# Optimization experiments

Measured on AMD Instinct MI355X. Metric: run time of the kernel, lower is better.

The kernel has to match this reference:

```python
import jax, jax.numpy as jnp
import numpy as np

B, T, IN, H, L, OUT = 1024, 48, 64, 512, 3, 1


def setup_inputs() -> dict:
    key = jax.random.key(0)
    ks = jax.random.split(key, 12)
    s = 0.05
    inp = {
        "x": jax.random.normal(ks[0], (B, T, IN), dtype=jnp.float32),
        # layer 0: input IN -> H ; gates concatenated [f,i,c,o] along last dim
        "Wx0": jax.random.normal(ks[1], (IN, 4 * H), dtype=jnp.float32) * s,
        "Wh0": jax.random.normal(ks[2], (H, 4 * H), dtype=jnp.float32) * s,
        "b0": jnp.zeros((4 * H,), dtype=jnp.float32),
        "Wx1": jax.random.normal(ks[3], (H, 4 * H), dtype=jnp.float32) * s,
        "Wh1": jax.random.normal(ks[4], (H, 4 * H), dtype=jnp.float32) * s,
        "b1": jnp.zeros((4 * H,), dtype=jnp.float32),
        "Wx2": jax.random.normal(ks[5], (H, 4 * H), dtype=jnp.float32) * s,
        "Wh2": jax.random.normal(ks[6], (H, 4 * H), dtype=jnp.float32) * s,
        "b2": jnp.zeros((4 * H,), dtype=jnp.float32),
        "fc_w": jax.random.normal(ks[7], (H, OUT), dtype=jnp.float32) * s,
        "fc_b": jnp.zeros((OUT,), dtype=jnp.float32),
    }
    return inp


def _lstm_cell(Wx, Wh, b, x_t, h, C):
    # fused 4-gate GEMM, same math as 8 separate Linears in the torch code
    g = x_t @ Wx + h @ Wh + b  # [B, 4H]
    f, i, c, o = jnp.split(g, 4, axis=-1)
    f = jax.nn.sigmoid(f)
    i = jax.nn.sigmoid(i)
    c = jnp.tanh(c)
    o = jax.nn.sigmoid(o)
    C_new = f * C + i * c
    h_new = o * jnp.tanh(C_new)  # dropout is identity in eval mode
    return h_new, C_new


def reference(x, Wx0, Wh0, b0, Wx1, Wh1, b1, Wx2, Wh2, b2, fc_w, fc_b):
    params = [(Wx0, Wh0, b0), (Wx1, Wh1, b1), (Wx2, Wh2, b2)]
    Bsz = x.shape[0]
    Hsz = Wh0.shape[0]
    h0 = jnp.zeros((L, Bsz, Hsz), dtype=x.dtype)
    C0 = jnp.zeros((L, Bsz, Hsz), dtype=x.dtype)

    def step(carry, x_t):
        h, C = carry
        inp = x_t
        hs, Cs = [], []
        for l in range(L):
            Wx, Wh, b = params[l]
            hn, Cn = _lstm_cell(Wx, Wh, b, inp, h[l], C[l])
            hs.append(hn)
            Cs.append(Cn)
            inp = hn
        return (jnp.stack(hs), jnp.stack(Cs)), None

    (h, C), _ = jax.lax.scan(step, (h0, C0), jnp.swapaxes(x, 0, 1))
    return h[-1] @ fc_w + fc_b  # [B, OUT]
```

## Files before the change

kernel.cpp:

```cpp
#include <hip/hip_runtime.h>
#include <hip/hip_bf16.h>
#include <stdint.h>

#define BSZ 1024
#define HSZ 512
#define TSZ 48
#define INSZ 64
#define GSZ 2048

typedef __attribute__((ext_vector_type(8))) short bf16x8;
typedef __attribute__((ext_vector_type(16))) float f32x16;

#define GLDS16(g, l)                                                        \
    __builtin_amdgcn_global_load_lds(                                       \
        (const __attribute__((address_space(1))) void*)(g),                 \
        (__attribute__((address_space(3))) void*)(l), 16, 0, 0)

__device__ __forceinline__ float sigmf(float x) { return 1.0f / (1.0f + __expf(-x)); }
__device__ __forceinline__ float tanhf_(float x) { return 2.0f / (1.0f + __expf(-2.0f * x)) - 1.0f; }

__global__ __launch_bounds__(256, 3) void lstm_diag(
    const __hip_bfloat16* __restrict__ xth, const __hip_bfloat16* __restrict__ xtl,
    __hip_bfloat16* __restrict__ hbuf,
    float* __restrict__ Cbuf,
    const __hip_bfloat16* __restrict__ W0h, const __hip_bfloat16* __restrict__ W0l,
    const __hip_bfloat16* __restrict__ W1h, const __hip_bfloat16* __restrict__ W1l,
    const __hip_bfloat16* __restrict__ W2h, const __hip_bfloat16* __restrict__ W2l,
    const float* __restrict__ b0, const float* __restrict__ b1,
    const float* __restrict__ b2,
    int d, int lmin)
{
    __shared__ __align__(16) char lds[49152];
    char* ldsAh = lds;
    char* ldsAl = lds + 8192;
    char* ldsBh = lds + 16384;
    char* ldsBl = lds + 32768;

    const int l = lmin + blockIdx.z;
    const int t = d - l;
    const size_t slab = (size_t)BSZ * HSZ;
    auto Hb = [&](int par, int ll, int hilo) {
        return hbuf + (((size_t)par * 3 + ll) * 2 + hilo) * slab;
    };

    const __hip_bfloat16* Wth = (l == 0) ? W0h : (l == 1) ? W1h : W2h;
    const __hip_bfloat16* Wtl = (l == 0) ? W0l : (l == 1) ? W1l : W2l;
    const float* bias = (l == 0) ? b0 : (l == 1) ? b1 : b2;
    const int Kx   = (l == 0) ? INSZ : HSZ;
    const int KCax = (l == 0) ? 8 : 64;
    const int Ktot = Kx + HSZ;
    const int KCt  = Ktot >> 3;
    const int nkx  = Kx >> 6;
    const int nkt  = Ktot >> 6;
    const int cur = t & 1, prv = cur ^ 1;
    const __hip_bfloat16* Axh = (l == 0) ? xth + (size_t)t * BSZ * INSZ : Hb(cur, l - 1, 0);
    const __hip_bfloat16* Axl = (l == 0) ? xtl + (size_t)t * BSZ * INSZ : Hb(cur, l - 1, 1);
    const __hip_bfloat16* Ahh = Hb(prv, l, 0);
    const __hip_bfloat16* Ahl = Hb(prv, l, 1);
    float* C = Cbuf + (size_t)l * slab;
    __hip_bfloat16* hhi = Hb(cur, l, 0);
    __hip_bfloat16* hlo = Hb(cur, l, 1);

    const int bid = blockIdx.x + (blockIdx.y << 4);
    const int swz = (bid & 7) * 32 + (bid >> 3);
    const int m0 = (swz & 15) * 64;
    const int n0 = (swz >> 4) * 128;
    const int p  = swz & 15;
    const int np = swz >> 4;

    const int tid = threadIdx.x;
    const int lane = tid & 63;
    const int wv = tid >> 6;
    const int lrow32 = lane & 31;
    const int lk2 = lane >> 5;

    int offA[2][4], offB[4];
#pragma unroll
    for (int mf = 0; mf < 2; ++mf)
#pragma unroll
        for (int ks = 0; ks < 4; ++ks)
            offA[mf][ks] = (ks * 2 + lk2) * 1024 + (mf * 32 + lrow32) * 16;
#pragma unroll
    for (int ks = 0; ks < 4; ++ks)
        offB[ks] = (ks * 2 + lk2) * 2048 + (wv * 32 + lrow32) * 16;

    f32x16 acc[2];
#pragma unroll
    for (int mf = 0; mf < 2; ++mf)
#pragma unroll
        for (int r = 0; r < 16; ++r) acc[mf][r] = 0.0f;

    auto stage = [&](const __hip_bfloat16* sh, const __hip_bfloat16* sl,
                     int KCa, int kcA0, int kcW0) {
#pragma unroll
        for (int i = 0; i < 2; ++i) {
            int sa = wv * 2 + i;
            size_t ro = ((size_t)p * KCa + kcA0 + sa) * 512 + lane * 8;
            GLDS16(sh + ro, ldsAh + sa * 1024);
            GLDS16(sl + ro, ldsAl + sa * 1024);
        }
#pragma unroll
        for (int i = 0; i < 4; ++i) {
            int sb = wv * 4 + i;
            size_t ro = ((size_t)np * KCt + kcW0 + (sb >> 1)) * 1024 + (sb & 1) * 512 + lane * 8;
            GLDS16(Wth + ro, ldsBh + sb * 1024);
            GLDS16(Wtl + ro, ldsBl + sb * 1024);
        }
    };

#pragma unroll 1
    for (int ks = 0; ks < nkt; ++ks) {
        __syncthreads();
        if (ks < nkx) stage(Axh, Axl, KCax, ks * 8, ks * 8);
        else          stage(Ahh, Ahl, 64, (ks - nkx) * 8, ks * 8);
        __syncthreads();
#pragma unroll
        for (int ksub = 0; ksub < 4; ++ksub) {
            bf16x8 ah0 = *(const bf16x8*)(ldsAh + offA[0][ksub]);
            bf16x8 ah1 = *(const bf16x8*)(ldsAh + offA[1][ksub]);
            bf16x8 al0 = *(const bf16x8*)(ldsAl + offA[0][ksub]);
            bf16x8 al1 = *(const bf16x8*)(ldsAl + offA[1][ksub]);
            bf16x8 bh  = *(const bf16x8*)(ldsBh + offB[ksub]);
            bf16x8 bl  = *(const bf16x8*)(ldsBl + offB[ksub]);
            acc[0] = __builtin_amdgcn_mfma_f32_32x32x16_bf16(ah0, bh, acc[0], 0, 0, 0);
            acc[1] = __builtin_amdgcn_mfma_f32_32x32x16_bf16(ah1, bh, acc[1], 0, 0, 0);
            acc[0] = __builtin_amdgcn_mfma_f32_32x32x16_bf16(al0, bh, acc[0], 0, 0, 0);
            acc[1] = __builtin_amdgcn_mfma_f32_32x32x16_bf16(al1, bh, acc[1], 0, 0, 0);
            acc[0] = __builtin_amdgcn_mfma_f32_32x32x16_bf16(ah0, bl, acc[0], 0, 0, 0);
            acc[1] = __builtin_amdgcn_mfma_f32_32x32x16_bf16(ah1, bl, acc[1], 0, 0, 0);
        }
    }

    __syncthreads();
    float* gt = (float*)lds;
#pragma unroll
    for (int mf = 0; mf < 2; ++mf)
#pragma unroll
        for (int rg = 0; rg < 16; ++rg) {
            int row = mf * 32 + (rg & 3) + 8 * (rg >> 2) + 4 * lk2;
            gt[row * 132 + wv * 32 + lrow32] = acc[mf][rg];
        }
    __syncthreads();

    const int n_l = tid & 31;
    const int rb2 = (tid >> 5) * 8;
    const int n_g = (n0 >> 2) + n_l;
    const int kc_h = n_g >> 3, e_h = n_g & 7;
    const float bf = bias[n_g], bi = bias[HSZ + n_g];
    const float bc = bias[2 * HSZ + n_g], bo = bias[3 * HSZ + n_g];
#pragma unroll
    for (int r = 0; r < 8; ++r) {
        int row = rb2 + r;
        int rg = m0 + row;
        float4 g4 = *(const float4*)&gt[row * 132 + n_l * 4];
        float f = sigmf(g4.x + bf);
        float i_ = sigmf(g4.y + bi);
        float c_ = tanhf_(g4.z + bc);
        float o_ = sigmf(g4.w + bo);
        size_t cidx = (size_t)rg * HSZ + n_g;
        float Cn = f * C[cidx] + i_ * c_;
        C[cidx] = Cn;
        float hv = o_ * tanhf_(Cn);
        __hip_bfloat16 hh = __float2bfloat16(hv);
        size_t hidx = (((size_t)(rg >> 6) * 64 + kc_h) * 64 + (rg & 63)) * 8 + e_h;
        hhi[hidx] = hh;
        hlo[hidx] = __float2bfloat16(hv - __bfloat162float(hh));
    }
}

__global__ __launch_bounds__(256) void convert_x(const float* __restrict__ x,
                                                 __hip_bfloat16* __restrict__ xh,
                                                 __hip_bfloat16* __restrict__ xl)
{
    int gid = blockIdx.x * 256 + threadIdx.x;
    int kc = gid & 7;
    int rem = gid >> 3;
    int r = rem & 63; rem >>= 6;
    int pp = rem & 15;
    int t = rem >> 4;
    int b = pp * 64 + r;
    const float* src = x + ((size_t)b * TSZ + t) * INSZ + kc * 8;
    short hi8[8], lo8[8];
#pragma unroll
    for (int e = 0; e < 8; ++e) {
        float v = src[e];
        __hip_bfloat16 h = __float2bfloat16(v);
        hi8[e] = *(short*)&h;
        __hip_bfloat16 lo = __float2bfloat16(v - __bfloat162float(h));
        lo8[e] = *(short*)&lo;
    }
    size_t o = ((((size_t)t * 16 + pp) * 8 + kc) * 64 + r) * 8;
    *(bf16x8*)((__hip_bfloat16*)xh + o) = *(bf16x8*)hi8;
    *(bf16x8*)((__hip_bfloat16*)xl + o) = *(bf16x8*)lo8;
}

__global__ __launch_bounds__(256) void convert_w(
    const float* __restrict__ Wx, const float* __restrict__ Wh, int Kx, int Ktot,
    __hip_bfloat16* __restrict__ outh, __hip_bfloat16* __restrict__ outl)
{
    __shared__ float tile[64][129];
    const int kt = blockIdx.x, np = blockIdx.y;
    const int k0 = kt * 64;
    const float* src;
    int krel;
    if (k0 < Kx) { src = Wx; krel = k0; } else { src = Wh; krel = k0 - Kx; }
#pragma unroll
    for (int i = 0; i < 32; ++i) {
        int idx = threadIdx.x + i * 256;
        int k_l = idx >> 7, gate = (idx >> 5) & 3, n_l = idx & 31;
        tile[k_l][n_l * 4 + gate] = src[(size_t)(krel + k_l) * GSZ + gate * HSZ + np * 32 + n_l];
    }
    __syncthreads();
    const size_t obase = ((size_t)np * (Ktot >> 3) + kt * 8) * 1024;
#pragma unroll
    for (int i = 0; i < 32; ++i) {
        int idx = threadIdx.x + i * 256;
        int kcl = idx >> 10, c = (idx >> 3) & 127, e = idx & 7;
        float v = tile[kcl * 8 + e][c];
        __hip_bfloat16 h = __float2bfloat16(v);
        outh[obase + idx] = h;
        outl[obase + idx] = __float2bfloat16(v - __bfloat162float(h));
    }
}

__global__ __launch_bounds__(256) void fc_kernel(
    const __hip_bfloat16* __restrict__ hh, const __hip_bfloat16* __restrict__ hl,
    const float* __restrict__ w, const float* __restrict__ b, float* __restrict__ out)
{
    int wave = (blockIdx.x * 256 + threadIdx.x) >> 6;
    int lane = threadIdx.x & 63;
    if (wave >= BSZ) return;
    int pp = wave >> 6, r = wave & 63;
    size_t o = (((size_t)pp * 64 + lane) * 64 + r) * 8;
    bf16x8 vh = *(const bf16x8*)(hh + o);
    bf16x8 vl = *(const bf16x8*)(hl + o);
    float s = 0.0f;
#pragma unroll
    for (int e = 0; e < 8; ++e) {
        ushort uh = (ushort)vh[e], ul = (ushort)vl[e];
        __hip_bfloat16 bh = *(__hip_bfloat16*)&uh;
        __hip_bfloat16 bl = *(__hip_bfloat16*)&ul;
        s += (__bfloat162float(bh) + __bfloat162float(bl)) * w[lane * 8 + e];
    }
#pragma unroll
    for (int off = 32; off; off >>= 1) s += __shfl_down(s, off);
    if (lane == 0) out[wave] = s + b[0];
}

extern "C" void kernel_launch(void* const* d_in, const int* in_sizes, int n_in,
                              void* d_out, int out_size, void* d_ws, size_t ws_size,
                              hipStream_t stream) {
    const float* x   = (const float*)d_in[0];
    const float* Wx0 = (const float*)d_in[1];
    const float* Wh0 = (const float*)d_in[2];
    const float* b0  = (const float*)d_in[3];
    const float* Wx1 = (const float*)d_in[4];
    const float* Wh1 = (const float*)d_in[5];
    const float* b1  = (const float*)d_in[6];
    const float* Wx2 = (const float*)d_in[7];
    const float* Wh2 = (const float*)d_in[8];
    const float* b2  = (const float*)d_in[9];
    const float* fcw = (const float*)d_in[10];
    const float* fcb = (const float*)d_in[11];

    char* p = (char*)d_ws;
    const size_t hslab = (size_t)BSZ * HSZ * sizeof(__hip_bfloat16);
    __hip_bfloat16* hbuf = (__hip_bfloat16*)p;
    p += 12 * hslab;
    float* Cbuf = (float*)p;
    p += 3 * (size_t)BSZ * HSZ * sizeof(float);
    const size_t zero_bytes = (size_t)(p - (char*)d_ws);

    const size_t xslab = (size_t)TSZ * BSZ * INSZ * sizeof(__hip_bfloat16);
    __hip_bfloat16* xth = (__hip_bfloat16*)p; p += xslab;
    __hip_bfloat16* xtl = (__hip_bfloat16*)p; p += xslab;

    const int K0 = INSZ + HSZ;
    const int K12 = 2 * HSZ;
    const size_t w0s = (size_t)GSZ * K0 * sizeof(__hip_bfloat16);
    const size_t w12s = (size_t)GSZ * K12 * sizeof(__hip_bfloat16);
    __hip_bfloat16* w0h = (__hip_bfloat16*)p; p += w0s;
    __hip_bfloat16* w0l = (__hip_bfloat16*)p; p += w0s;
    __hip_bfloat16* w1h = (__hip_bfloat16*)p; p += w12s;
    __hip_bfloat16* w1l = (__hip_bfloat16*)p; p += w12s;
    __hip_bfloat16* w2h = (__hip_bfloat16*)p; p += w12s;
    __hip_bfloat16* w2l = (__hip_bfloat16*)p; p += w12s;

    hipMemsetAsync(d_ws, 0, zero_bytes, stream);

    convert_x<<<dim3(TSZ * BSZ * 8 / 256), dim3(256), 0, stream>>>(x, xth, xtl);
    convert_w<<<dim3(K0 / 64, 16), dim3(256), 0, stream>>>(Wx0, Wh0, INSZ, K0, w0h, w0l);
    convert_w<<<dim3(K12 / 64, 16), dim3(256), 0, stream>>>(Wx1, Wh1, HSZ, K12, w1h, w1l);
    convert_w<<<dim3(K12 / 64, 16), dim3(256), 0, stream>>>(Wx2, Wh2, HSZ, K12, w2h, w2l);

    for (int dgn = 0; dgn < TSZ + 2; ++dgn) {
        int lmin = (dgn - (TSZ - 1)) > 0 ? (dgn - (TSZ - 1)) : 0;
        int lmax = dgn < 2 ? dgn : 2;
        int ncells = lmax - lmin + 1;
        lstm_diag<<<dim3(16, 16, ncells), dim3(256), 0, stream>>>(
            xth, xtl, hbuf, Cbuf,
            w0h, w0l, w1h, w1l, w2h, w2l,
            b0, b1, b2, dgn, lmin);
    }

    __hip_bfloat16* h2h = hbuf + (((size_t)1 * 3 + 2) * 2 + 0) * BSZ * HSZ;
    __hip_bfloat16* h2l = hbuf + (((size_t)1 * 3 + 2) * 2 + 1) * BSZ * HSZ;
    fc_kernel<<<dim3(BSZ / 4), dim3(256), 0, stream>>>(h2h, h2l, fcw, fcb, (float*)d_out);
}
```

Baseline: 2.042 ms.

## Replace LDS-staged GEMM mainloop with direct global-to-register prefetch pipeline

```diff
diff --git a/kernel.cpp b/kernel.cpp
--- a/kernel.cpp
+++ b/kernel.cpp
@@ -10,11 +10,6 @@
 
 typedef __attribute__((ext_vector_type(8))) short bf16x8;
 typedef __attribute__((ext_vector_type(16))) float f32x16;
-
-#define GLDS16(g, l)                                                        \
-    __builtin_amdgcn_global_load_lds(                                       \
-        (const __attribute__((address_space(1))) void*)(g),                 \
-        (__attribute__((address_space(3))) void*)(l), 16, 0, 0)
 
 __device__ __forceinline__ float sigmf(float x) { return 1.0f / (1.0f + __expf(-x)); }
 __device__ __forceinline__ float tanhf_(float x) { return 2.0f / (1.0f + __expf(-2.0f * x)) - 1.0f; }
@@ -30,11 +25,7 @@
     const float* __restrict__ b2,
     int d, int lmin)
 {
-    __shared__ __align__(16) char lds[49152];
-    char* ldsAh = lds;
-    char* ldsAl = lds + 8192;
-    char* ldsBh = lds + 16384;
-    char* ldsBl = lds + 32768;
+    __shared__ __align__(16) float gt[64 * 132];
 
     const int l = lmin + blockIdx.z;
     const int t = d - l;
@@ -50,8 +41,8 @@
     const int KCax = (l == 0) ? 8 : 64;
     const int Ktot = Kx + HSZ;
     const int KCt  = Ktot >> 3;
-    const int nkx  = Kx >> 6;
-    const int nkt  = Ktot >> 6;
+    const int qx   = Kx >> 4;
+    const int qtot = Ktot >> 4;
     const int cur = t & 1, prv = cur ^ 1;
     const __hip_bfloat16* Axh = (l == 0) ? xth + (size_t)t * BSZ * INSZ : Hb(cur, l - 1, 0);
     const __hip_bfloat16* Axl = (l == 0) ? xtl + (size_t)t * BSZ * INSZ : Hb(cur, l - 1, 1);
@@ -74,72 +65,64 @@
     const int lrow32 = lane & 31;
     const int lk2 = lane >> 5;
 
-    int offA[2][4], offB[4];
-#pragma unroll
-    for (int mf = 0; mf < 2; ++mf)
-#pragma unroll
-        for (int ks = 0; ks < 4; ++ks)
-            offA[mf][ks] = (ks * 2 + lk2) * 1024 + (mf * 32 + lrow32) * 16;
-#pragma unroll
-    for (int ks = 0; ks < 4; ++ks)
-        offB[ks] = (ks * 2 + lk2) * 2048 + (wv * 32 + lrow32) * 16;
-
-    f32x16 acc[2];
-#pragma unroll
-    for (int mf = 0; mf < 2; ++mf)
-#pragma unroll
-        for (int r = 0; r < 16; ++r) acc[mf][r] = 0.0f;
-
-    auto stage = [&](const __hip_bfloat16* sh, const __hip_bfloat16* sl,
-                     int KCa, int kcA0, int kcW0) {
-#pragma unroll
-        for (int i = 0; i < 2; ++i) {
-            int sa = wv * 2 + i;
-            size_t ro = ((size_t)p * KCa + kcA0 + sa) * 512 + lane * 8;
-            GLDS16(sh + ro, ldsAh + sa * 1024);
-            GLDS16(sl + ro, ldsAl + sa * 1024);
-        }
-#pragma unroll
-        for (int i = 0; i < 4; ++i) {
-            int sb = wv * 4 + i;
-            size_t ro = ((size_t)np * KCt + kcW0 + (sb >> 1)) * 1024 + (sb & 1) * 512 + lane * 8;
-            GLDS16(Wth + ro, ldsBh + sb * 1024);
-            GLDS16(Wtl + ro, ldsBl + sb * 1024);
-        }
-    };
+    const char* bAxh = (const char*)Axh + (size_t)p * KCax * 1024;
+    const char* bAxl = (const char*)Axl + (size_t)p * KCax * 1024;
+    const char* bAhh = (const char*)Ahh + (size_t)p * 64 * 1024;
+    const char* bAhl = (const char*)Ahl + (size_t)p * 64 * 1024;
+    const char* bWh  = (const char*)Wth + (size_t)np * KCt * 2048;
+    const char* bWl  = (const char*)Wtl + (size_t)np * KCt * 2048;
+
+    const int aoff = lk2 * 1024 + lrow32 * 16;
+    const int boff = lk2 * 2048 + (wv * 32 + lrow32) * 16;
+
+    f32x16 acc0, acc1;
+#pragma unroll
+    for (int r = 0; r < 16; ++r) { acc0[r] = 0.0f; acc1[r] = 0.0f; }
+
+    bf16x8 ah[4][2], al[4][2], bhv[4], blv[4];
+
+#define LOAD_SLOT(S, Q)                                                       \
+    { const int q_ = (Q);                                                     \
+      const char *pah, *pal;                                                  \
+      if (q_ < qx) { pah = bAxh + q_ * 2048; pal = bAxl + q_ * 2048; }        \
+      else { pah = bAhh + (q_ - qx) * 2048; pal = bAhl + (q_ - qx) * 2048; }  \
+      ah[S][0] = *(const bf16x8*)(pah + aoff);                                \
+      ah[S][1] = *(const bf16x8*)(pah + aoff + 512);                          \
+      al[S][0] = *(const bf16x8*)(pal + aoff);                                \
+      al[S][1] = *(const bf16x8*)(pal + aoff + 512);                          \
+      bhv[S] = __builtin_nontemporal_load((const bf16x8*)(bWh + q_ * 4096 + boff)); \
+      blv[S] = __builtin_nontemporal_load((const bf16x8*)(bWl + q_ * 4096 + boff)); }
+
+#define MMA_SLOT(S)                                                           \
+    acc0 = __builtin_amdgcn_mfma_f32_32x32x16_bf16(ah[S][0], bhv[S], acc0, 0, 0, 0); \
+    acc1 = __builtin_amdgcn_mfma_f32_32x32x16_bf16(ah[S][1], bhv[S], acc1, 0, 0, 0); \
+    acc0 = __builtin_amdgcn_mfma_f32_32x32x16_bf16(al[S][0], bhv[S], acc0, 0, 0, 0); \
+    acc1 = __builtin_amdgcn_mfma_f32_32x32x16_bf16(al[S][1], bhv[S], acc1, 0, 0, 0); \
+    acc0 = __builtin_amdgcn_mfma_f32_32x32x16_bf16(ah[S][0], blv[S], acc0, 0, 0, 0); \
+    acc1 = __builtin_amdgcn_mfma_f32_32x32x16_bf16(ah[S][1], blv[S], acc1, 0, 0, 0);
+
+    LOAD_SLOT(0, 0)
+    LOAD_SLOT(1, 1)
+    LOAD_SLOT(2, 2)
+    LOAD_SLOT(3, 3)
 
 #pragma unroll 1
-    for (int ks = 0; ks < nkt; ++ks) {
-        __syncthreads();
-        if (ks < nkx) stage(Axh, Axl, KCax, ks * 8, ks * 8);
-        else          stage(Ahh, Ahl, 64, (ks - nkx) * 8, ks * 8);
-        __syncthreads();
-#pragma unroll
-        for (int ksub = 0; ksub < 4; ++ksub) {
-            bf16x8 ah0 = *(const bf16x8*)(ldsAh + offA[0][ksub]);
-            bf16x8 ah1 = *(const bf16x8*)(ldsAh + offA[1][ksub]);
-            bf16x8 al0 = *(const bf16x8*)(ldsAl + offA[0][ksub]);
-            bf16x8 al1 = *(const bf16x8*)(ldsAl + offA[1][ksub]);
-            bf16x8 bh  = *(const bf16x8*)(ldsBh + offB[ksub]);
-            bf16x8 bl  = *(const bf16x8*)(ldsBl + offB[ksub]);
-            acc[0] = __builtin_amdgcn_mfma_f32_32x32x16_bf16(ah0, bh, acc[0], 0, 0, 0);
-            acc[1] = __builtin_amdgcn_mfma_f32_32x32x16_bf16(ah1, bh, acc[1], 0, 0, 0);
-            acc[0] = __builtin_amdgcn_mfma_f32_32x32x16_bf16(al0, bh, acc[0], 0, 0, 0);
-            acc[1] = __builtin_amdgcn_mfma_f32_32x32x16_bf16(al1, bh, acc[1], 0, 0, 0);
-            acc[0] = __builtin_amdgcn_mfma_f32_32x32x16_bf16(ah0, bl, acc[0], 0, 0, 0);
-            acc[1] = __builtin_amdgcn_mfma_f32_32x32x16_bf16(ah1, bl, acc[1], 0, 0, 0);
-        }
-    }
+    for (int qq = 0; qq < qtot; qq += 4) {
+        MMA_SLOT(0) if (qq + 4 < qtot) LOAD_SLOT(0, qq + 4)
+        MMA_SLOT(1) if (qq + 5 < qtot) LOAD_SLOT(1, qq + 5)
+        MMA_SLOT(2) if (qq + 6 < qtot) LOAD_SLOT(2, qq + 6)
+        MMA_SLOT(3) if (qq + 7 < qtot) LOAD_SLOT(3, qq + 7)
+    }
+#undef LOAD_SLOT
+#undef MMA_SLOT
 
     __syncthreads();
-    float* gt = (float*)lds;
-#pragma unroll
-    for (int mf = 0; mf < 2; ++mf)
-#pragma unroll
-        for (int rg = 0; rg < 16; ++rg) {
-            int row = mf * 32 + (rg & 3) + 8 * (rg >> 2) + 4 * lk2;
-            gt[row * 132 + wv * 32 + lrow32] = acc[mf][rg];
-        }
+#pragma unroll
+    for (int rg = 0; rg < 16; ++rg) {
+        int row0 = (rg & 3) + 8 * (rg >> 2) + 4 * lk2;
+        gt[row0 * 132 + wv * 32 + lrow32] = acc0[rg];
+        gt[(row0 + 32) * 132 + wv * 32 + lrow32] = acc1[rg];
+    }
     __syncthreads();
 
     const int n_l = tid & 31;
```

After: 2.925 ms. 1.43x slower.

## Double-buffer activation tiles in LDS and load weights directly to registers

Applied to the files above, without the earlier changes.

```diff
diff --git a/kernel.cpp b/kernel.cpp
--- a/kernel.cpp
+++ b/kernel.cpp
@@ -30,11 +30,7 @@
     const float* __restrict__ b2,
     int d, int lmin)
 {
-    __shared__ __align__(16) char lds[49152];
-    char* ldsAh = lds;
-    char* ldsAl = lds + 8192;
-    char* ldsBh = lds + 16384;
-    char* ldsBl = lds + 32768;
+    __shared__ __align__(16) char lds[33792];
 
     const int l = lmin + blockIdx.z;
     const int t = d - l;
@@ -74,72 +70,87 @@
     const int lrow32 = lane & 31;
     const int lk2 = lane >> 5;
 
-    int offA[2][4], offB[4];
-#pragma unroll
-    for (int mf = 0; mf < 2; ++mf)
-#pragma unroll
-        for (int ks = 0; ks < 4; ++ks)
-            offA[mf][ks] = (ks * 2 + lk2) * 1024 + (mf * 32 + lrow32) * 16;
-#pragma unroll
-    for (int ks = 0; ks < 4; ++ks)
-        offB[ks] = (ks * 2 + lk2) * 2048 + (wv * 32 + lrow32) * 16;
-
-    f32x16 acc[2];
-#pragma unroll
-    for (int mf = 0; mf < 2; ++mf)
-#pragma unroll
-        for (int r = 0; r < 16; ++r) acc[mf][r] = 0.0f;
-
-    auto stage = [&](const __hip_bfloat16* sh, const __hip_bfloat16* sl,
-                     int KCa, int kcA0, int kcW0) {
+    const int r0  = (wv >> 1) * 32;
+    const int c0w = (wv & 1) * 64;
+
+    const char* bAxh = (const char*)Axh + (size_t)p * KCax * 1024;
+    const char* bAxl = (const char*)Axl + (size_t)p * KCax * 1024;
+    const char* bAhh = (const char*)Ahh + (size_t)p * 64 * 1024;
+    const char* bAhl = (const char*)Ahl + (size_t)p * 64 * 1024;
+    const char* bWh = (const char*)Wth + (size_t)np * KCt * 2048;
+    const char* bWl = (const char*)Wtl + (size_t)np * KCt * 2048;
+
+    const int aoff = (r0 + lrow32) * 16;
+    const int boff = (c0w + lrow32) * 16;
+
+    f32x16 acc0, acc1;
+#pragma unroll
+    for (int r = 0; r < 16; ++r) { acc0[r] = 0.0f; acc1[r] = 0.0f; }
+
+    auto stage = [&](int ks) {
+        const char *sh, *sl;
+        int kc0;
+        if (ks < nkx) { sh = bAxh; sl = bAxl; kc0 = ks * 8; }
+        else          { sh = bAhh; sl = bAhl; kc0 = (ks - nkx) * 8; }
+        char* dst = lds + (ks & 1) * 16384;
 #pragma unroll
         for (int i = 0; i < 2; ++i) {
-            int sa = wv * 2 + i;
-            size_t ro = ((size_t)p * KCa + kcA0 + sa) * 512 + lane * 8;
-            GLDS16(sh + ro, ldsAh + sa * 1024);
-            GLDS16(sl + ro, ldsAl + sa * 1024);
-        }
-#pragma unroll
-        for (int i = 0; i < 4; ++i) {
-            int sb = wv * 4 + i;
-            size_t ro = ((size_t)np * KCt + kcW0 + (sb >> 1)) * 1024 + (sb & 1) * 512 + lane * 8;
-            GLDS16(Wth + ro, ldsBh + sb * 1024);
-            GLDS16(Wtl + ro, ldsBl + sb * 1024);
+            int kc = wv * 2 + i;
+            size_t so = (size_t)(kc0 + kc) * 1024 + lane * 16;
+            GLDS16(sh + so, dst + kc * 1024);
+            GLDS16(sl + so, dst + 8192 + kc * 1024);
         }
     };
+
+    stage(0);
 
 #pragma unroll 1
     for (int ks = 0; ks < nkt; ++ks) {
         __syncthreads();
-        if (ks < nkx) stage(Axh, Axl, KCax, ks * 8, ks * 8);
-        else          stage(Ahh, Ahl, 64, (ks - nkx) * 8, ks * 8);
-        __syncthreads();
-#pragma unroll
-        for (int ksub = 0; ksub < 4; ++ksub) {
-            bf16x8 ah0 = *(const bf16x8*)(ldsAh + offA[0][ksub]);
-            bf16x8 ah1 = *(const bf16x8*)(ldsAh + offA[1][ksub]);
-            bf16x8 al0 = *(const bf16x8*)(ldsAl + offA[0][ksub]);
-            bf16x8 al1 = *(const bf16x8*)(ldsAl + offA[1][ksub]);
-            bf16x8 bh  = *(const bf16x8*)(ldsBh + offB[ksub]);
-            bf16x8 bl  = *(const bf16x8*)(ldsBl + offB[ksub]);
-            acc[0] = __builtin_amdgcn_mfma_f32_32x32x16_bf16(ah0, bh, acc[0], 0, 0, 0);
-            acc[1] = __builtin_amdgcn_mfma_f32_32x32x16_bf16(ah1, bh, acc[1], 0, 0, 0);
-            acc[0] = __builtin_amdgcn_mfma_f32_32x32x16_bf16(al0, bh, acc[0], 0, 0, 0);
-            acc[1] = __builtin_amdgcn_mfma_f32_32x32x16_bf16(al1, bh, acc[1], 0, 0, 0);
-            acc[0] = __builtin_amdgcn_mfma_f32_32x32x16_bf16(ah0, bl, acc[0], 0, 0, 0);
-            acc[1] = __builtin_amdgcn_mfma_f32_32x32x16_bf16(ah1, bl, acc[1], 0, 0, 0);
+
+        bf16x8 bh[4][2], bl[4][2];
+        {
+            const char* wb = bWh + (size_t)ks * 16384;
+            const char* wl = bWl + (size_t)ks * 16384;
+#pragma unroll
+            for (int s = 0; s < 4; ++s) {
+                int ko = (s * 2 + lk2) * 2048;
+                bh[s][0] = *(const bf16x8*)(wb + ko + boff);
+                bh[s][1] = *(const bf16x8*)(wb + ko + boff + 512);
+                bl[s][0] = *(const bf16x8*)(wl + ko + boff);
+                bl[s][1] = *(const bf16x8*)(wl + ko + boff + 512);
+            }
         }
+        __builtin_amdgcn_sched_barrier(0);
+
+        if (ks + 1 < nkt) stage(ks + 1);
+        __builtin_amdgcn_sched_barrier(0);
+
+        char* bufb = lds + (ks & 1) * 16384;
+        __builtin_amdgcn_s_setprio(1);
+#pragma unroll
+        for (int s = 0; s < 4; ++s) {
+            int ao = (s * 2 + lk2) * 1024 + aoff;
+            bf16x8 ahv = *(const bf16x8*)(bufb + ao);
+            bf16x8 alv = *(const bf16x8*)(bufb + 8192 + ao);
+            acc0 = __builtin_amdgcn_mfma_f32_32x32x16_bf16(ahv, bh[s][0], acc0, 0, 0, 0);
+            acc1 = __builtin_amdgcn_mfma_f32_32x32x16_bf16(ahv, bh[s][1], acc1, 0, 0, 0);
+            acc0 = __builtin_amdgcn_mfma_f32_32x32x16_bf16(alv, bh[s][0], acc0, 0, 0, 0);
+            acc1 = __builtin_amdgcn_mfma_f32_32x32x16_bf16(alv, bh[s][1], acc1, 0, 0, 0);
+            acc0 = __builtin_amdgcn_mfma_f32_32x32x16_bf16(ahv, bl[s][0], acc0, 0, 0, 0);
+            acc1 = __builtin_amdgcn_mfma_f32_32x32x16_bf16(ahv, bl[s][1], acc1, 0, 0, 0);
+        }
+        __builtin_amdgcn_s_setprio(0);
     }
 
     __syncthreads();
     float* gt = (float*)lds;
 #pragma unroll
-    for (int mf = 0; mf < 2; ++mf)
-#pragma unroll
-        for (int rg = 0; rg < 16; ++rg) {
-            int row = mf * 32 + (rg & 3) + 8 * (rg >> 2) + 4 * lk2;
-            gt[row * 132 + wv * 32 + lrow32] = acc[mf][rg];
-        }
+    for (int rg = 0; rg < 16; ++rg) {
+        int row = r0 + (rg & 3) + 8 * (rg >> 2) + 4 * lk2;
+        gt[row * 132 + c0w + lrow32] = acc0[rg];
+        gt[row * 132 + c0w + 32 + lrow32] = acc1[rg];
+    }
     __syncthreads();
 
     const int n_l = tid & 31;
```

Result: slower. 2.226 ms (+9.0%).
